# Optimization experiments

Measured on AMD Instinct MI355X. Metric: run time of the kernel, lower is better.

Reference implementation:

```python
import jax, jax.numpy as jnp
import numpy as np
import math

B, S, HID = 1, 2048, 2048
NH, NKV, HD = 32, 8, 64
GROUPS = NH // NKV
BOOST_SCALE, NARROW_SCALE = 1.0, 4.0
NEG = -1e9


def rope_cos_sin(seq_len, scale):
    inv_freq = 1.0 / (10000.0 ** (jnp.arange(0, HD, 2, dtype=jnp.float32) / HD))
    t = jnp.arange(seq_len, dtype=jnp.float32) / scale
    freqs = jnp.outer(t, inv_freq)                      # [s, hd/2]
    emb = jnp.concatenate([freqs, freqs], axis=-1)      # [s, hd]
    return jnp.cos(emb), jnp.sin(emb)


def rotate_half(x):
    x1, x2 = x[..., : HD // 2], x[..., HD // 2:]
    return jnp.concatenate([-x2, x1], axis=-1)


def apply_rope(q, k, cos, sin, position_ids):
    c = cos[position_ids][:, None]                      # [b,1,s,hd]
    s = sin[position_ids][:, None]
    return q * c + rotate_half(q) * s, k * c + rotate_half(k) * s


def setup_inputs() -> dict:
    key = jax.random.key(0)
    ks = jax.random.split(key, 5)
    hidden_states = jax.random.normal(ks[0], (B, S, HID), dtype=jnp.float32)
    i = jnp.arange(S)[:, None]
    j = jnp.arange(S)[None, :]
    attention_mask = jnp.where(j <= i, 0.0, NEG).astype(jnp.float32)[None, None]  # [1,1,S,S]
    position_ids = jnp.broadcast_to(jnp.arange(S, dtype=jnp.int32)[None], (B, S))
    sc = 1.0 / math.sqrt(HID)
    Wq = jax.random.normal(ks[1], (NH * HD, HID), dtype=jnp.float32) * sc
    Wk = jax.random.normal(ks[2], (NKV * HD, HID), dtype=jnp.float32) * sc
    Wv = jax.random.normal(ks[3], (NKV * HD, HID), dtype=jnp.float32) * sc
    Wo = jax.random.normal(ks[4], (HID, HID), dtype=jnp.float32) * sc
    return dict(hidden_states=hidden_states, attention_mask=attention_mask,
                position_ids=position_ids, Wq=Wq, Wk=Wk, Wv=Wv, Wo=Wo)


def reference(hidden_states, attention_mask, position_ids, Wq, Wk, Wv, Wo):
    b, q_len, _ = hidden_states.shape
    kv_seq_len = q_len

    q = (hidden_states @ Wq.T).reshape(b, q_len, NH, HD).transpose(0, 2, 1, 3)   # [b,H,s,hd]
    k = (hidden_states @ Wk.T).reshape(b, q_len, NKV, HD).transpose(0, 2, 1, 3)  # [b,Hkv,s,hd]
    v = (hidden_states @ Wv.T).reshape(b, q_len, NKV, HD).transpose(0, 2, 1, 3)

    boost_cos, boost_sin = rope_cos_sin(kv_seq_len, BOOST_SCALE)
    narrow_cos, narrow_sin = rope_cos_sin(kv_seq_len + 30, NARROW_SCALE)
    bq, bk = apply_rope(q, k, boost_cos, boost_sin, position_ids)
    nq, nk = apply_rope(q, k, narrow_cos, narrow_sin, position_ids)

    # repeat_kv (GQA)
    bk = jnp.repeat(bk, GROUPS, axis=1)
    nk = jnp.repeat(nk, GROUPS, axis=1)
    v = jnp.repeat(v, GROUPS, axis=1)

    inv_sqrt = 1.0 / math.sqrt(HD)
    big = jnp.einsum('bhqd,bhkd->bhqk', bq, bk) * inv_sqrt
    small = jnp.einsum('bhqd,bhkd->bhqk', nq, nk) * inv_sqrt
    big = big + attention_mask
    small = small + attention_mask

    # neighbor mask: tril minus (for rows >= context_length) tril(diag=context_length)
    # which zeroes those rows entirely -> neighbor = (j <= i) & (i < context_length)
    context_length = q_len - 10
    i = jnp.arange(q_len)[:, None]
    j = jnp.arange(kv_seq_len)[None, :]
    neighbor = (j <= i) & (i < context_length)

    merged = jnp.where(neighbor, big, small)
    probs = jax.nn.softmax(merged.astype(jnp.float32), axis=-1).astype(q.dtype)
    attn = jnp.einsum('bhqk,bhkd->bhqd', probs, v)
    attn = attn.transpose(0, 2, 1, 3).reshape(b, q_len, HID)
    return attn @ Wo.T
```

## Files before the change

### kernel.cpp

```cpp
#include <hip/hip_runtime.h>
#include <math.h>

#define S_LEN 2048
#define HIDN  2048
#define NH    32
#define NKV   8
#define HD    64
#define KVW   (NKV * HD)
#define CTX   (S_LEN - 10)

typedef unsigned short u16;
typedef __attribute__((ext_vector_type(4))) float f32x4;
typedef __attribute__((ext_vector_type(16))) float f32x16;
typedef __attribute__((ext_vector_type(8))) short s16x8;

#define QSCL 0.18033688011112042f
#define L2_1E4 13.287712379549449f

__device__ __forceinline__ float bf2f(u16 u) {
  union { unsigned int i; float f; } v; v.i = ((unsigned int)u) << 16; return v.f;
}
__device__ __forceinline__ u16 f2bf(float f) {
  union { float f; unsigned int i; } v; v.f = f;
  unsigned int r = v.i + 0x7fffu + ((v.i >> 16) & 1u);
  return (u16)(r >> 16);
}
__device__ __forceinline__ unsigned int cvt_pk_bf16(float a, float b) {
  unsigned int d;
  asm("v_cvt_pk_bf16_f32 %0, %1, %2" : "=v"(d) : "v"(a), "v"(b));
  return d;
}

__global__ __launch_bounds__(256) void conv_all(
    const float* __restrict__ h,  const float* __restrict__ wq,
    const float* __restrict__ wk, const float* __restrict__ wv,
    const float* __restrict__ wo,
    u16* __restrict__ Hb, u16* __restrict__ Wqb, u16* __restrict__ Wkb,
    u16* __restrict__ Wvb, u16* __restrict__ Wob)
{
  const int i = blockIdx.x * 256 + threadIdx.x;
  const float* src; u16* dst; int off;
  if      (i < 1048576) { src = h;  dst = Hb;  off = i; }
  else if (i < 2097152) { src = wq; dst = Wqb; off = i - 1048576; }
  else if (i < 2359296) { src = wk; dst = Wkb; off = i - 2097152; }
  else if (i < 2621440) { src = wv; dst = Wvb; off = i - 2359296; }
  else                  { src = wo; dst = Wob; off = i - 2621440; }
  const float4 f4 = ((const float4*)src)[off];
  ushort4 o4;
  o4.x = f2bf(f4.x); o4.y = f2bf(f4.y); o4.z = f2bf(f4.z); o4.w = f2bf(f4.w);
  ((ushort4*)dst)[off] = o4;
}

#define BM 128
#define BN 128
#define BK 64

template<int MODE>
__device__ __forceinline__ void gemm_body(
    u16* __restrict__ As, u16* __restrict__ Bs,
    const u16* __restrict__ A, const u16* __restrict__ B,
    void* __restrict__ Cv, void* __restrict__ Cv2,
    int N, int K, int row0, int col0, const int* __restrict__ pos)
{
  const int tid  = threadIdx.x;
  const int wave = tid >> 6;
  const int lane = tid & 63;
  const int wr = (wave >> 1) * 64;
  const int wc = (wave & 1) * 64;

  f32x4 acc[4][4] = {};

  const int srow = wave * 8 + (lane >> 3);
  const int scol = (lane & 7) * 8;
  const int NT = K / BK;

#pragma unroll
  for (int it = 0; it < 4; ++it) {
    const u16* gA = A + (size_t)(row0 + it * 32 + srow) * K + scol;
    const u16* gB = B + (size_t)(col0 + it * 32 + srow) * K + scol;
    u16* lA = As + (it * 32 + wave * 8) * BK;
    u16* lB = Bs + (it * 32 + wave * 8) * BK;
    __builtin_amdgcn_global_load_lds((const __attribute__((address_space(1))) void*)gA,
                                     (__attribute__((address_space(3))) void*)lA, 16, 0, 0);
    __builtin_amdgcn_global_load_lds((const __attribute__((address_space(1))) void*)gB,
                                     (__attribute__((address_space(3))) void*)lB, 16, 0, 0);
  }

  int cur = 0;
  for (int t = 0; t < NT; ++t) {
    __builtin_amdgcn_s_barrier();
    __builtin_amdgcn_sched_barrier(0);
    if (t + 1 < NT) {
      const int kt = (t + 1) * BK;
      const int nx = (cur ^ 1) * (BM * BK);
#pragma unroll
      for (int it = 0; it < 4; ++it) {
        const u16* gA = A + (size_t)(row0 + it * 32 + srow) * K + kt + scol;
        const u16* gB = B + (size_t)(col0 + it * 32 + srow) * K + kt + scol;
        u16* lA = As + nx + (it * 32 + wave * 8) * BK;
        u16* lB = Bs + nx + (it * 32 + wave * 8) * BK;
        __builtin_amdgcn_global_load_lds((const __attribute__((address_space(1))) void*)gA,
                                         (__attribute__((address_space(3))) void*)lA, 16, 0, 0);
        __builtin_amdgcn_global_load_lds((const __attribute__((address_space(1))) void*)gB,
                                         (__attribute__((address_space(3))) void*)lB, 16, 0, 0);
      }
      asm volatile("s_waitcnt vmcnt(8)" ::: "memory");
    } else {
      asm volatile("s_waitcnt vmcnt(0)" ::: "memory");
    }
    __builtin_amdgcn_sched_barrier(0);
    __builtin_amdgcn_s_barrier();
    __builtin_amdgcn_sched_barrier(0);

    const u16* Asb = As + cur * (BM * BK);
    const u16* Bsb = Bs + cur * (BM * BK);
#pragma unroll
    for (int kk = 0; kk < 2; ++kk) {
      const int ko = kk * 32 + (lane >> 4) * 8;
      s16x8 af[4], bg[4];
#pragma unroll
      for (int mi = 0; mi < 4; ++mi)
        af[mi] = *(const s16x8*)&Asb[(wr + mi * 16 + (lane & 15)) * BK + ko];
#pragma unroll
      for (int ni = 0; ni < 4; ++ni)
        bg[ni] = *(const s16x8*)&Bsb[(wc + ni * 16 + (lane & 15)) * BK + ko];
#pragma unroll
      for (int mi = 0; mi < 4; ++mi)
#pragma unroll
        for (int ni = 0; ni < 4; ++ni)
          acc[mi][ni] = __builtin_amdgcn_mfma_f32_16x16x32_bf16(af[mi], bg[ni], acc[mi][ni], 0, 0, 0);
    }
    cur ^= 1;
  }

  const int rq = (lane >> 4) * 4;
  const int cq = lane & 15;

  if (MODE == 3) {
#pragma unroll
    for (int mi = 0; mi < 4; ++mi)
#pragma unroll
      for (int ni = 0; ni < 4; ++ni) {
        const int r = row0 + wr + mi * 16 + rq;
        const int c = col0 + wc + ni * 16 + cq;
#pragma unroll
        for (int t = 0; t < 4; ++t)
          ((float*)Cv)[(size_t)(r + t) * N + c] = acc[mi][ni][t];
      }
  } else if (MODE == 2) {
#pragma unroll
    for (int mi = 0; mi < 4; ++mi)
#pragma unroll
      for (int ni = 0; ni < 4; ++ni) {
        const int r = row0 + wr + mi * 16 + rq;
        const int c = col0 + wc + ni * 16 + cq;
        ushort4 o4;
        o4.x = f2bf(acc[mi][ni][0]); o4.y = f2bf(acc[mi][ni][1]);
        o4.z = f2bf(acc[mi][ni][2]); o4.w = f2bf(acc[mi][ni][3]);
        *(ushort4*)&((u16*)Cv)[(size_t)c * S_LEN + r] = o4;
      }
  } else {
#pragma unroll
    for (int mi = 0; mi < 4; ++mi) {
#pragma unroll
      for (int t = 0; t < 4; ++t) {
        const int i = row0 + wr + mi * 16 + rq + t;
        const float fpos = (float)pos[i];
#pragma unroll
        for (int ni = 0; ni < 2; ++ni) {
          const int d = ni * 16 + cq;
          const int c = col0 + wc + ni * 16 + cq;
          const float f = exp2f(-(float)(2 * d) * (1.0f / HD) * L2_1E4);
          const float x1 = acc[mi][ni][t], x2 = acc[mi][ni + 2][t];
          if (MODE == 0) {
            const float scl = (i < CTX) ? 1.0f : 0.25f;
            float sn, cs; sincosf(fpos * scl * f, &sn, &cs);
            u16* Cq = (u16*)Cv;
            Cq[(size_t)i * N + c]      = f2bf((x1 * cs - x2 * sn) * QSCL);
            Cq[(size_t)i * N + c + 32] = f2bf((x2 * cs + x1 * sn) * QSCL);
          } else {
            float sb_, cb_; sincosf(fpos * f, &sb_, &cb_);
            float sn_, cn_; sincosf(fpos * 0.25f * f, &sn_, &cn_);
            u16* Kb_ = (u16*)Cv;
            u16* Kn_ = (u16*)Cv2;
            Kb_[(size_t)i * N + c]      = f2bf(x1 * cb_ - x2 * sb_);
            Kb_[(size_t)i * N + c + 32] = f2bf(x2 * cb_ + x1 * sb_);
            Kn_[(size_t)i * N + c]      = f2bf(x1 * cn_ - x2 * sn_);
            Kn_[(size_t)i * N + c + 32] = f2bf(x2 * cn_ + x1 * sn_);
          }
        }
      }
    }
  }
}

__global__ __launch_bounds__(256) void gemm_qkv(
    const u16* __restrict__ A, const u16* __restrict__ Wq, const u16* __restrict__ Wk,
    const u16* __restrict__ Wv, u16* __restrict__ Q, u16* __restrict__ Kb,
    u16* __restrict__ Kn, u16* __restrict__ Vt, const int* __restrict__ pos)
{
  __shared__ u16 As[2 * BM * BK];
  __shared__ u16 Bs[2 * BN * BK];
  const int bn = blockIdx.x;
  const int row0 = blockIdx.y * BM;
  if (bn < 16)
    gemm_body<0>(As, Bs, A, Wq, Q, nullptr, HIDN, HIDN, row0, bn * BN, pos);
  else if (bn < 20)
    gemm_body<1>(As, Bs, A, Wk, Kb, Kn, KVW, HIDN, row0, (bn - 16) * BN, pos);
  else
    gemm_body<2>(As, Bs, A, Wv, Vt, nullptr, KVW, HIDN, row0, (bn - 20) * BN, pos);
}

__global__ __launch_bounds__(256) void gemm_out(
    const u16* __restrict__ A, const u16* __restrict__ B, float* __restrict__ C, int N, int K)
{
  __shared__ u16 As[2 * BM * BK];
  __shared__ u16 Bs[2 * BN * BK];
  gemm_body<3>(As, Bs, A, B, C, nullptr, N, K, blockIdx.y * BM, blockIdx.x * BN, nullptr);
}

#define PAD 8
__global__ __launch_bounds__(256) void attn_mfma(
    const u16* __restrict__ Q, const u16* __restrict__ K, const u16* __restrict__ Kn,
    const u16* __restrict__ Vt, u16* __restrict__ O)
{
  __shared__ __align__(16) u16 Ks[64][HD + PAD];
  __shared__ __align__(16) u16 Kns[64][HD + PAD];
  __shared__ __align__(16) u16 Vts[HD][64 + PAD];
  __shared__ __align__(16) float Of[64][64];
  __shared__ float Lf[2][32];
  __shared__ float Li[2][32];

  const int tid  = threadIdx.x;
  const int wave = tid >> 6;
  const int lane = tid & 63;
  const int l31  = lane & 31;
  const int hi   = lane >> 5;
  const int wr   = wave >> 1;
  const int wk   = wave & 1;
  const int h    = blockIdx.y;
  const int kh   = h >> 2;
  const int pr   = blockIdx.x;

  int sa[2], sb[2];
#pragma unroll
  for (int it = 0; it < 2; ++it) {
    const int u = it * 256 + tid;
    sa[it] = u >> 3;
    sb[it] = (u & 7) * 8;
  }

  for (int ph = 0; ph < 2; ++ph) {
    const int qt = ph ? pr : 31 - pr;
    const int i_base = qt * 64;
    const int rw0 = i_base + wr * 32;
    const bool mixed_blk = (qt == 31);
    const bool mixed_wv  = mixed_blk && (rw0 + 31 >= CTX);

    s16x8 bq[4];
#pragma unroll
    for (int i = 0; i < 4; ++i)
      bq[i] = *(const s16x8*)(Q + (size_t)(rw0 + l31) * HIDN + h * HD + i * 16 + hi * 8);

    f32x16 acc0 = {};
    f32x16 acc1 = {};
    float lsum = 0.f;

    const int ntiles = qt + 1;
    s16x8 kr[2], vr[2], knr[2];
#pragma unroll
    for (int it = 0; it < 2; ++it) {
      kr[it] = *(const s16x8*)(K  + (size_t)sa[it] * KVW + kh * HD + sb[it]);
      vr[it] = *(const s16x8*)(Vt + (size_t)(kh * HD + sa[it]) * S_LEN + sb[it]);
      if (mixed_blk) knr[it] = *(const s16x8*)(Kn + (size_t)sa[it] * KVW + kh * HD + sb[it]);
    }

    for (int t = 0; t < ntiles; ++t) {
      const int jt = t * 64;
      __syncthreads();
#pragma unroll
      for (int it = 0; it < 2; ++it) {
        *(s16x8*)&Ks[sa[it]][sb[it]]  = kr[it];
        *(s16x8*)&Vts[sa[it]][sb[it]] = vr[it];
        if (mixed_blk) *(s16x8*)&Kns[sa[it]][sb[it]] = knr[it];
      }
      __syncthreads();
      if (t + 1 < ntiles) {
        const int jn = jt + 64;
#pragma unroll
        for (int it = 0; it < 2; ++it) {
          kr[it] = *(const s16x8*)(K  + (size_t)(jn + sa[it]) * KVW + kh * HD + sb[it]);
          vr[it] = *(const s16x8*)(Vt + (size_t)(kh * HD + sa[it]) * S_LEN + jn + sb[it]);
          if (mixed_blk) knr[it] = *(const s16x8*)(Kn + (size_t)(jn + sa[it]) * KVW + kh * HD + sb[it]);
        }
      }

      const int j0 = jt + wk * 32;
      if (j0 > rw0 + 31) continue;
      const bool needmask = (j0 + 31 > rw0);

      f32x16 sc = {};
#pragma unroll
      for (int i = 0; i < 4; ++i) {
        const s16x8 ak = *(const s16x8*)&Ks[wk * 32 + l31][i * 16 + hi * 8];
        sc = __builtin_amdgcn_mfma_f32_32x32x16_bf16(ak, bq[i], sc, 0, 0, 0);
      }
      if (mixed_wv) {
        f32x16 scn = {};
#pragma unroll
        for (int i = 0; i < 4; ++i) {
          const s16x8 ak = *(const s16x8*)&Kns[wk * 32 + l31][i * 16 + hi * 8];
          scn = __builtin_amdgcn_mfma_f32_32x32x16_bf16(ak, bq[i], scn, 0, 0, 0);
        }
        const bool nar = (rw0 + l31) >= CTX;
#pragma unroll
        for (int r = 0; r < 16; ++r) sc[r] = nar ? scn[r] : sc[r];
      }

      float p[16];
#pragma unroll
      for (int r = 0; r < 16; ++r) {
        float e = __builtin_amdgcn_exp2f(fminf(sc[r], 80.f));
        if (needmask) {
          const int key = j0 + (r & 3) + 8 * (r >> 2) + 4 * hi;
          e = (key > rw0 + l31) ? 0.f : e;
        }
        p[r] = e;
        lsum += e;
      }

      unsigned int c[4][2];
#pragma unroll
      for (int blk = 0; blk < 4; ++blk) {
        c[blk][0] = cvt_pk_bf16(p[4 * blk + 0], p[4 * blk + 1]);
        c[blk][1] = cvt_pk_bf16(p[4 * blk + 2], p[4 * blk + 3]);
      }

#pragma unroll
      for (int s = 0; s < 2; ++s) {
        unsigned int w0 = c[2 * s][0], w2 = c[2 * s + 1][0];
        unsigned int w1 = c[2 * s][1], w3 = c[2 * s + 1][1];
        asm("v_permlane32_swap_b32 %0, %1" : "+v"(w0), "+v"(w2));
        asm("v_permlane32_swap_b32 %0, %1" : "+v"(w1), "+v"(w3));
        union { unsigned int u[4]; s16x8 v; } af;
        af.u[0] = w0; af.u[1] = w1; af.u[2] = w2; af.u[3] = w3;
        const int kc = wk * 32 + s * 16 + hi * 8;
        const s16x8 v0 = *(const s16x8*)&Vts[l31][kc];
        const s16x8 v1 = *(const s16x8*)&Vts[32 + l31][kc];
        acc0 = __builtin_amdgcn_mfma_f32_32x32x16_bf16(af.v, v0, acc0, 0, 0, 0);
        acc1 = __builtin_amdgcn_mfma_f32_32x32x16_bf16(af.v, v1, acc1, 0, 0, 0);
      }
    }

    lsum += __shfl_xor(lsum, 32, 64);
    __syncthreads();
    if (wk == 1) {
#pragma unroll
      for (int r = 0; r < 16; ++r) {
        const int rl = (r & 3) + 8 * (r >> 2) + 4 * hi;
        Of[wr * 32 + rl][l31]      = acc0[r];
        Of[wr * 32 + rl][l31 + 32] = acc1[r];
      }
      if (hi == 0) Lf[wr][l31] = lsum;
    }
    __syncthreads();
    if (wk == 0) {
      const float tot = lsum + Lf[wr][l31];
      const float inv = 1.0f / fmaxf(tot, 1e-30f);
      if (hi == 0) Li[wr][l31] = inv;
#pragma unroll
      for (int r = 0; r < 16; ++r) {
        const int rl = (r & 3) + 8 * (r >> 2) + 4 * hi;
        const float iv = Li[wr][rl];
        const size_t o = (size_t)(rw0 + rl) * HIDN + h * HD + l31;
        O[o]      = f2bf((acc0[r] + Of[wr * 32 + rl][l31])      * iv);
        O[o + 32] = f2bf((acc1[r] + Of[wr * 32 + rl][l31 + 32]) * iv);
      }
    }
  }
}

extern "C" void kernel_launch(void* const* d_in, const int* in_sizes, int n_in,
                              void* d_out, int out_size, void* d_ws, size_t ws_size,
                              hipStream_t stream)
{
  const float* hidden = (const float*)d_in[0];
  const int* pos      = (const int*)d_in[2];
  const float* Wq = (const float*)d_in[3];
  const float* Wk = (const float*)d_in[4];
  const float* Wv = (const float*)d_in[5];
  const float* Wo = (const float*)d_in[6];
  float* out = (float*)d_out;

  char* ws = (char*)d_ws;
  u16* Qb  = (u16*)(ws);
  u16* Kbb = (u16*)(ws + (8u  << 20));
  u16* Knb = (u16*)(ws + (10u << 20));
  u16* Vtb = (u16*)(ws + (12u << 20));
  u16* Ab  = (u16*)(ws + (14u << 20));
  u16* Hb  = (u16*)(ws + (22u << 20));
  u16* Wqb = (u16*)(ws + (30u << 20));
  u16* Wkb = (u16*)(ws + (38u << 20));
  u16* Wvb = (u16*)(ws + (40u << 20));
  u16* Wob = (u16*)(ws + (42u << 20));

  conv_all<<<dim3(14336), 256, 0, stream>>>(hidden, Wq, Wk, Wv, Wo, Hb, Wqb, Wkb, Wvb, Wob);
  gemm_qkv<<<dim3(24, 16), 256, 0, stream>>>(Hb, Wqb, Wkb, Wvb, Qb, Kbb, Knb, Vtb, pos);
  attn_mfma<<<dim3(16, NH), 256, 0, stream>>>(Qb, Kbb, Knb, Vtb, Ab);
  gemm_out<<<dim3(16, 16), 256, 0, stream>>>(Ab, Wob, out, HIDN, HIDN);
}
```

Before: 274.1 us.

## Shrink GEMM N-tile to 64, drop double buffering, use fast trig in RoPE

Halves the GEMM output tile width so each wave computes a 32x64 slab. This doubles the block count for the QKV and output projections, which should balance work better across the CUs. It also replaces the double-buffered asynchronous LDS prefetch with a single buffer guarded by two __syncthreads per K step, which frees LDS but stops overlapping loads with MFMA work. The RoPE epilogue switches from sincosf to the __sinf/__cosf intrinsics, which are cheaper but may lose accuracy at large angles.

```diff
diff --git a/kernel.cpp b/kernel.cpp
--- a/kernel.cpp
+++ b/kernel.cpp
@@ -52,7 +52,7 @@
 }
 
 #define BM 128
-#define BN 128
+#define BN 64
 #define BK 64
 
 template<int MODE>
@@ -65,95 +65,70 @@
   const int tid  = threadIdx.x;
   const int wave = tid >> 6;
   const int lane = tid & 63;
-  const int wr = (wave >> 1) * 64;
-  const int wc = (wave & 1) * 64;
-
-  f32x4 acc[4][4] = {};
+  const int l15  = lane & 15;
+  const int wr   = wave * 32;
+
+  f32x4 acc[2][4] = {};
 
   const int srow = wave * 8 + (lane >> 3);
   const int scol = (lane & 7) * 8;
-  const int NT = K / BK;
-
-#pragma unroll
-  for (int it = 0; it < 4; ++it) {
-    const u16* gA = A + (size_t)(row0 + it * 32 + srow) * K + scol;
-    const u16* gB = B + (size_t)(col0 + it * 32 + srow) * K + scol;
-    u16* lA = As + (it * 32 + wave * 8) * BK;
-    u16* lB = Bs + (it * 32 + wave * 8) * BK;
-    __builtin_amdgcn_global_load_lds((const __attribute__((address_space(1))) void*)gA,
-                                     (__attribute__((address_space(3))) void*)lA, 16, 0, 0);
-    __builtin_amdgcn_global_load_lds((const __attribute__((address_space(1))) void*)gB,
-                                     (__attribute__((address_space(3))) void*)lB, 16, 0, 0);
-  }
-
-  int cur = 0;
-  for (int t = 0; t < NT; ++t) {
-    __builtin_amdgcn_s_barrier();
-    __builtin_amdgcn_sched_barrier(0);
-    if (t + 1 < NT) {
-      const int kt = (t + 1) * BK;
-      const int nx = (cur ^ 1) * (BM * BK);
-#pragma unroll
-      for (int it = 0; it < 4; ++it) {
-        const u16* gA = A + (size_t)(row0 + it * 32 + srow) * K + kt + scol;
-        const u16* gB = B + (size_t)(col0 + it * 32 + srow) * K + kt + scol;
-        u16* lA = As + nx + (it * 32 + wave * 8) * BK;
-        u16* lB = Bs + nx + (it * 32 + wave * 8) * BK;
-        __builtin_amdgcn_global_load_lds((const __attribute__((address_space(1))) void*)gA,
-                                         (__attribute__((address_space(3))) void*)lA, 16, 0, 0);
-        __builtin_amdgcn_global_load_lds((const __attribute__((address_space(1))) void*)gB,
-                                         (__attribute__((address_space(3))) void*)lB, 16, 0, 0);
-      }
-      asm volatile("s_waitcnt vmcnt(8)" ::: "memory");
-    } else {
-      asm volatile("s_waitcnt vmcnt(0)" ::: "memory");
-    }
-    __builtin_amdgcn_sched_barrier(0);
-    __builtin_amdgcn_s_barrier();
-    __builtin_amdgcn_sched_barrier(0);
-
-    const u16* Asb = As + cur * (BM * BK);
-    const u16* Bsb = Bs + cur * (BM * BK);
+
+  for (int kt = 0; kt < K; kt += BK) {
+#pragma unroll
+    for (int it = 0; it < 4; ++it) {
+      const u16* gA = A + (size_t)(row0 + it * 32 + srow) * K + kt + scol;
+      u16* lA = &As[(it * 32 + wave * 8) * BK];
+      __builtin_amdgcn_global_load_lds((const __attribute__((address_space(1))) void*)gA,
+                                       (__attribute__((address_space(3))) void*)lA, 16, 0, 0);
+    }
+#pragma unroll
+    for (int it = 0; it < 2; ++it) {
+      const u16* gB = B + (size_t)(col0 + it * 32 + srow) * K + kt + scol;
+      u16* lB = &Bs[(it * 32 + wave * 8) * BK];
+      __builtin_amdgcn_global_load_lds((const __attribute__((address_space(1))) void*)gB,
+                                       (__attribute__((address_space(3))) void*)lB, 16, 0, 0);
+    }
+    __syncthreads();
 #pragma unroll
     for (int kk = 0; kk < 2; ++kk) {
       const int ko = kk * 32 + (lane >> 4) * 8;
-      s16x8 af[4], bg[4];
-#pragma unroll
-      for (int mi = 0; mi < 4; ++mi)
-        af[mi] = *(const s16x8*)&Asb[(wr + mi * 16 + (lane & 15)) * BK + ko];
+      s16x8 af[2], bg[4];
+#pragma unroll
+      for (int mi = 0; mi < 2; ++mi)
+        af[mi] = *(const s16x8*)&As[(wr + mi * 16 + l15) * BK + ko];
 #pragma unroll
       for (int ni = 0; ni < 4; ++ni)
-        bg[ni] = *(const s16x8*)&Bsb[(wc + ni * 16 + (lane & 15)) * BK + ko];
-#pragma unroll
-      for (int mi = 0; mi < 4; ++mi)
+        bg[ni] = *(const s16x8*)&Bs[(ni * 16 + l15) * BK + ko];
+#pragma unroll
+      for (int mi = 0; mi < 2; ++mi)
 #pragma unroll
         for (int ni = 0; ni < 4; ++ni)
           acc[mi][ni] = __builtin_amdgcn_mfma_f32_16x16x32_bf16(af[mi], bg[ni], acc[mi][ni], 0, 0, 0);
     }
-    cur ^= 1;
+    __syncthreads();
   }
 
   const int rq = (lane >> 4) * 4;
-  const int cq = lane & 15;
+  const int cq = l15;
 
   if (MODE == 3) {
 #pragma unroll
-    for (int mi = 0; mi < 4; ++mi)
+    for (int mi = 0; mi < 2; ++mi)
 #pragma unroll
       for (int ni = 0; ni < 4; ++ni) {
         const int r = row0 + wr + mi * 16 + rq;
-        const int c = col0 + wc + ni * 16 + cq;
+        const int c = col0 + ni * 16 + cq;
 #pragma unroll
         for (int t = 0; t < 4; ++t)
           ((float*)Cv)[(size_t)(r + t) * N + c] = acc[mi][ni][t];
       }
   } else if (MODE == 2) {
 #pragma unroll
-    for (int mi = 0; mi < 4; ++mi)
+    for (int mi = 0; mi < 2; ++mi)
 #pragma unroll
       for (int ni = 0; ni < 4; ++ni) {
         const int r = row0 + wr + mi * 16 + rq;
-        const int c = col0 + wc + ni * 16 + cq;
+        const int c = col0 + ni * 16 + cq;
         ushort4 o4;
         o4.x = f2bf(acc[mi][ni][0]); o4.y = f2bf(acc[mi][ni][1]);
         o4.z = f2bf(acc[mi][ni][2]); o4.w = f2bf(acc[mi][ni][3]);
@@ -161,7 +136,7 @@
       }
   } else {
 #pragma unroll
-    for (int mi = 0; mi < 4; ++mi) {
+    for (int mi = 0; mi < 2; ++mi) {
 #pragma unroll
       for (int t = 0; t < 4; ++t) {
         const int i = row0 + wr + mi * 16 + rq + t;
@@ -169,24 +144,24 @@
 #pragma unroll
         for (int ni = 0; ni < 2; ++ni) {
           const int d = ni * 16 + cq;
-          const int c = col0 + wc + ni * 16 + cq;
+          const int c = col0 + d;
           const float f = exp2f(-(float)(2 * d) * (1.0f / HD) * L2_1E4);
           const float x1 = acc[mi][ni][t], x2 = acc[mi][ni + 2][t];
           if (MODE == 0) {
             const float scl = (i < CTX) ? 1.0f : 0.25f;
-            float sn, cs; sincosf(fpos * scl * f, &sn, &cs);
+            const float a  = fpos * scl * f;
+            const float cs = __cosf(a), sn = __sinf(a);
             u16* Cq = (u16*)Cv;
             Cq[(size_t)i * N + c]      = f2bf((x1 * cs - x2 * sn) * QSCL);
             Cq[(size_t)i * N + c + 32] = f2bf((x2 * cs + x1 * sn) * QSCL);
           } else {
-            float sb_, cb_; sincosf(fpos * f, &sb_, &cb_);
-            float sn_, cn_; sincosf(fpos * 0.25f * f, &sn_, &cn_);
-            u16* Kb_ = (u16*)Cv;
-            u16* Kn_ = (u16*)Cv2;
-            Kb_[(size_t)i * N + c]      = f2bf(x1 * cb_ - x2 * sb_);
-            Kb_[(size_t)i * N + c + 32] = f2bf(x2 * cb_ + x1 * sb_);
-            Kn_[(size_t)i * N + c]      = f2bf(x1 * cn_ - x2 * sn_);
-            Kn_[(size_t)i * N + c + 32] = f2bf(x2 * cn_ + x1 * sn_);
+            const float ab = fpos * f, an = fpos * 0.25f * f;
+            const float cb_ = __cosf(ab), sb_ = __sinf(ab);
+            const float cn_ = __cosf(an), sn_ = __sinf(an);
+            ((u16*)Cv)[(size_t)i * N + c]       = f2bf(x1 * cb_ - x2 * sb_);
+            ((u16*)Cv)[(size_t)i * N + c + 32]  = f2bf(x2 * cb_ + x1 * sb_);
+            ((u16*)Cv2)[(size_t)i * N + c]      = f2bf(x1 * cn_ - x2 * sn_);
+            ((u16*)Cv2)[(size_t)i * N + c + 32] = f2bf(x2 * cn_ + x1 * sn_);
           }
         }
       }
@@ -199,23 +174,23 @@
     const u16* __restrict__ Wv, u16* __restrict__ Q, u16* __restrict__ Kb,
     u16* __restrict__ Kn, u16* __restrict__ Vt, const int* __restrict__ pos)
 {
-  __shared__ u16 As[2 * BM * BK];
-  __shared__ u16 Bs[2 * BN * BK];
+  __shared__ u16 As[BM * BK];
+  __shared__ u16 Bs[BN * BK];
   const int bn = blockIdx.x;
   const int row0 = blockIdx.y * BM;
-  if (bn < 16)
+  if (bn < 32)
     gemm_body<0>(As, Bs, A, Wq, Q, nullptr, HIDN, HIDN, row0, bn * BN, pos);
-  else if (bn < 20)
-    gemm_body<1>(As, Bs, A, Wk, Kb, Kn, KVW, HIDN, row0, (bn - 16) * BN, pos);
+  else if (bn < 40)
+    gemm_body<1>(As, Bs, A, Wk, Kb, Kn, KVW, HIDN, row0, (bn - 32) * BN, pos);
   else
-    gemm_body<2>(As, Bs, A, Wv, Vt, nullptr, KVW, HIDN, row0, (bn - 20) * BN, pos);
+    gemm_body<2>(As, Bs, A, Wv, Vt, nullptr, KVW, HIDN, row0, (bn - 40) * BN, pos);
 }
 
 __global__ __launch_bounds__(256) void gemm_out(
     const u16* __restrict__ A, const u16* __restrict__ B, float* __restrict__ C, int N, int K)
 {
-  __shared__ u16 As[2 * BM * BK];
-  __shared__ u16 Bs[2 * BN * BK];
+  __shared__ u16 As[BM * BK];
+  __shared__ u16 Bs[BN * BK];
   gemm_body<3>(As, Bs, A, B, C, nullptr, N, K, blockIdx.y * BM, blockIdx.x * BN, nullptr);
 }
 
@@ -405,7 +380,7 @@
   u16* Wob = (u16*)(ws + (42u << 20));
 
   conv_all<<<dim3(14336), 256, 0, stream>>>(hidden, Wq, Wk, Wv, Wo, Hb, Wqb, Wkb, Wvb, Wob);
-  gemm_qkv<<<dim3(24, 16), 256, 0, stream>>>(Hb, Wqb, Wkb, Wvb, Qb, Kbb, Knb, Vtb, pos);
+  gemm_qkv<<<dim3(48, 16), 256, 0, stream>>>(Hb, Wqb, Wkb, Wvb, Qb, Kbb, Knb, Vtb, pos);
   attn_mfma<<<dim3(16, NH), 256, 0, stream>>>(Qb, Kbb, Knb, Vtb, Ab);
-  gemm_out<<<dim3(16, 16), 256, 0, stream>>>(Ab, Wob, out, HIDN, HIDN);
-}
+  gemm_out<<<dim3(32, 16), 256, 0, stream>>>(Ab, Wob, out, HIDN, HIDN);
+}
```

Result: faster. 250.3 us (-8.7%).
